# Kernel optimization log

Hardware: AMD Instinct MI355X
Metric: run time of the kernel (lower is better)

The kernel has to match this reference:

```python
import jax, jax.numpy as jnp
import numpy as np

NUM_CLASSES = 10000
FEAT_DIM = 256
BATCH = 4096
CLAMP_MIN = 1e-12
CLAMP_MAX = 1e12


def setup_inputs() -> dict:
    key = jax.random.key(0)
    k1, k2, k3 = jax.random.split(key, 3)
    x = jax.random.normal(k1, (BATCH, FEAT_DIM), dtype=jnp.float32)
    labels = jax.random.randint(k2, (BATCH,), 0, NUM_CLASSES, dtype=jnp.int64)
    centers = jax.random.normal(k3, (NUM_CLASSES, FEAT_DIM), dtype=jnp.float32)
    return {"x": x, "labels": labels, "centers": centers}


def reference(x, labels, centers):
    # x: [B, D], labels: [B], centers: [C, D]
    B = x.shape[0]
    C = centers.shape[0]
    # distmat[b, c] = ||x_b||^2 + ||center_c||^2 - 2 <x_b, center_c>
    x2 = jnp.sum(x * x, axis=1, keepdims=True)            # [B, 1]
    c2 = jnp.sum(centers * centers, axis=1)[None, :]       # [1, C]
    distmat = x2 + c2 - 2.0 * jnp.einsum('bd,cd->bc', x, centers)  # [B, C]
    # one-hot mask selecting the matching-class column per row
    mask = (labels[:, None] == jnp.arange(C)[None, :]).astype(distmat.dtype)  # [B, C]
    dist = distmat * mask
    # NOTE: faithful to torch — clamp is applied AFTER masking, so the
    # (C-1) zeroed entries per row each contribute CLAMP_MIN to the sum.
    loss = jnp.clip(dist, CLAMP_MIN, CLAMP_MAX).sum() / B
    return loss
```

## Files before the change

kernel.cpp:

```cpp
#include <hip/hip_runtime.h>


#define BATCH      4096
#define FEAT_DIM   256
#define NUM_CLS    10000
#define CLAMP_MIN_F 1e-12f
#define CLAMP_MAX_F 1e12f

__global__ __launch_bounds__(256) void cmcl_row_dist(
    const float* __restrict__ x,
    const int*   __restrict__ labels,
    const float* __restrict__ centers,
    float*       __restrict__ partial)
{
    const int lane = threadIdx.x & 63;
    const int wave = threadIdx.x >> 6;
    const int row  = (blockIdx.x << 2) + wave;

    const int label = labels[row];
    const float4* __restrict__ xr = (const float4*)(x       + (size_t)row   * FEAT_DIM);
    const float4* __restrict__ cr = (const float4*)(centers + (size_t)label * FEAT_DIM);

    float4 xv = xr[lane];
    float4 cv = cr[lane];
    float dx = xv.x - cv.x;
    float dy = xv.y - cv.y;
    float dz = xv.z - cv.z;
    float dw = xv.w - cv.w;
    float v = dx*dx + dy*dy + dz*dz + dw*dw;

    #pragma unroll
    for (int off = 32; off > 0; off >>= 1)
        v += __shfl_down(v, off, 64);

    __shared__ float sm[4];
    if (lane == 0) {
        v = fminf(fmaxf(v, CLAMP_MIN_F), CLAMP_MAX_F);
        sm[wave] = v;
    }
    __syncthreads();
    if (threadIdx.x == 0)
        partial[blockIdx.x] = sm[0] + sm[1] + sm[2] + sm[3];
}

__global__ __launch_bounds__(256) void cmcl_reduce(
    const float* __restrict__ partial,
    float*       __restrict__ out)
{
    float v = partial[threadIdx.x]
            + partial[threadIdx.x + 256]
            + partial[threadIdx.x + 512]
            + partial[threadIdx.x + 768];

    #pragma unroll
    for (int off = 32; off > 0; off >>= 1)
        v += __shfl_down(v, off, 64);

    __shared__ float sm[4];
    const int lane = threadIdx.x & 63;
    const int wave = threadIdx.x >> 6;
    if (lane == 0) sm[wave] = v;
    __syncthreads();
    if (threadIdx.x == 0) {
        float total = sm[0] + sm[1] + sm[2] + sm[3];
        out[0] = total / (float)BATCH + (float)(NUM_CLS - 1) * CLAMP_MIN_F;
    }
}

extern "C" void kernel_launch(void* const* d_in, const int* in_sizes, int n_in,
                              void* d_out, int out_size, void* d_ws, size_t ws_size,
                              hipStream_t stream) {
    const float* x       = (const float*)d_in[0];
    const int*   labels  = (const int*)  d_in[1];
    const float* centers = (const float*)d_in[2];
    float*       out     = (float*)d_out;
    float*       partial = (float*)d_ws;

    cmcl_row_dist<<<BATCH / 4, 256, 0, stream>>>(x, labels, centers, partial);
    cmcl_reduce<<<1, 256, 0, stream>>>(partial, out);
}
```

Baseline: 65.60 us.

## Fuse row-distance and final reduction into one cooperative kernel with grid sync

Merges the two kernels into a single cooperative launch of 256 blocks, each handling 16 rows (4 per wave), then uses a grid-wide sync so block 0 reduces the 256 partials and writes the loss. This removes the second kernel launch and its gap, and cuts the partial count. In exchange it adds cooperative-launch overhead and a grid barrier, and gives each wave more serial work with less parallelism.

```diff
diff --git a/kernel.cpp b/kernel.cpp
--- a/kernel.cpp
+++ b/kernel.cpp
@@ -1,69 +1,69 @@
 #include <hip/hip_runtime.h>
+#include <hip/hip_cooperative_groups.h>
+
+namespace cg = cooperative_groups;
 
 
-#define BATCH      4096
-#define FEAT_DIM   256
-#define NUM_CLS    10000
+#define BATCH       4096
+#define FEAT_DIM    256
+#define NUM_CLS     10000
 #define CLAMP_MIN_F 1e-12f
 #define CLAMP_MAX_F 1e12f
 
-__global__ __launch_bounds__(256) void cmcl_row_dist(
+__global__ __launch_bounds__(256) void cmcl_fused(
     const float* __restrict__ x,
     const int*   __restrict__ labels,
     const float* __restrict__ centers,
-    float*       __restrict__ partial)
+    float*       __restrict__ partial,
+    float*       __restrict__ out)
 {
     const int lane = threadIdx.x & 63;
     const int wave = threadIdx.x >> 6;
-    const int row  = (blockIdx.x << 2) + wave;
 
-    const int label = labels[row];
-    const float4* __restrict__ xr = (const float4*)(x       + (size_t)row   * FEAT_DIM);
-    const float4* __restrict__ cr = (const float4*)(centers + (size_t)label * FEAT_DIM);
-
-    float4 xv = xr[lane];
-    float4 cv = cr[lane];
-    float dx = xv.x - cv.x;
-    float dy = xv.y - cv.y;
-    float dz = xv.z - cv.z;
-    float dw = xv.w - cv.w;
-    float v = dx*dx + dy*dy + dz*dz + dw*dw;
+    float acc = 0.0f;
 
     #pragma unroll
-    for (int off = 32; off > 0; off >>= 1)
-        v += __shfl_down(v, off, 64);
+    for (int i = 0; i < 4; ++i) {
+        const int row   = (blockIdx.x << 4) + (wave << 2) + i;
+        const int label = labels[row];
+
+        float4 xv = ((const float4*)(x       + (size_t)row   * FEAT_DIM))[lane];
+        float4 cv = ((const float4*)(centers + (size_t)label * FEAT_DIM))[lane];
+        float dx = xv.x - cv.x;
+        float dy = xv.y - cv.y;
+        float dz = xv.z - cv.z;
+        float dw = xv.w - cv.w;
+        float v = dx*dx + dy*dy + dz*dz + dw*dw;
+
+        #pragma unroll
+        for (int off = 32; off > 0; off >>= 1)
+            v += __shfl_down(v, off, 64);
+
+        if (lane == 0)
+            acc += fminf(fmaxf(v, CLAMP_MIN_F), CLAMP_MAX_F);
+    }
 
     __shared__ float sm[4];
-    if (lane == 0) {
-        v = fminf(fmaxf(v, CLAMP_MIN_F), CLAMP_MAX_F);
-        sm[wave] = v;
-    }
+    if (lane == 0) sm[wave] = acc;
     __syncthreads();
     if (threadIdx.x == 0)
         partial[blockIdx.x] = sm[0] + sm[1] + sm[2] + sm[3];
-}
 
-__global__ __launch_bounds__(256) void cmcl_reduce(
-    const float* __restrict__ partial,
-    float*       __restrict__ out)
-{
-    float v = partial[threadIdx.x]
-            + partial[threadIdx.x + 256]
-            + partial[threadIdx.x + 512]
-            + partial[threadIdx.x + 768];
+    cg::this_grid().sync();
 
-    #pragma unroll
-    for (int off = 32; off > 0; off >>= 1)
-        v += __shfl_down(v, off, 64);
+    if (blockIdx.x == 0) {
+        float v = partial[threadIdx.x];
+        #pragma unroll
+        for (int off = 32; off > 0; off >>= 1)
+            v += __shfl_down(v, off, 64);
 
-    __shared__ float sm[4];
-    const int lane = threadIdx.x & 63;
-    const int wave = threadIdx.x >> 6;
-    if (lane == 0) sm[wave] = v;
-    __syncthreads();
-    if (threadIdx.x == 0) {
-        float total = sm[0] + sm[1] + sm[2] + sm[3];
-        out[0] = total / (float)BATCH + (float)(NUM_CLS - 1) * CLAMP_MIN_F;
+        __shared__ float sm2[4];
+        if (lane == 0) sm2[wave] = v;
+        __syncthreads();
+        if (threadIdx.x == 0) {
+            float total = sm2[0] + sm2[1] + sm2[2] + sm2[3];
+            out[0] = total / (float)BATCH + (float)(NUM_CLS - 1) * CLAMP_MIN_F;
+        }
     }
 }
 
@@ -76,6 +76,8 @@
     float*       out     = (float*)d_out;
     float*       partial = (float*)d_ws;
 
-    cmcl_row_dist<<<BATCH / 4, 256, 0, stream>>>(x, labels, centers, partial);
-    cmcl_reduce<<<1, 256, 0, stream>>>(partial, out);
+    void* args[] = { (void*)&x, (void*)&labels, (void*)&centers,
+                     (void*)&partial, (void*)&out };
+    hipLaunchCooperativeKernel((void*)cmcl_fused, dim3(256), dim3(256),
+                               args, 0, stream);
 }
```

Result: slower. 102.0 us (+55.4%).
